# Optimization experiments

Measured on AMD Instinct MI355X. Metric: run time of the kernel, lower is better.

Reference implementation:

```python
import jax, jax.numpy as jnp
import numpy as np

B, T, D = 2, 1024, 2048
H, DK, DV = 32, 48, 96
KD, VD = H * DK, H * DV   # 1536, 3072
CS = 4
INTER = 5632
EPS = 1e-5


def rmsnorm(x, w, eps=EPS):
    return x * jax.lax.rsqrt(jnp.mean(x * x, axis=-1, keepdims=True) + eps) * w


def short_conv(x, w):
    # causal depthwise conv1d + silu; x [B,T,C], w [C,K]
    K = w.shape[1]
    xp = jnp.pad(x, ((0, 0), (K - 1, 0), (0, 0)))
    out = sum(xp[:, k:k + x.shape[1], :] * w[:, k] for k in range(K))
    return jax.nn.silu(out)


def l2norm(x, eps=1e-6):
    return x * jax.lax.rsqrt(jnp.sum(x * x, axis=-1, keepdims=True) + eps)


def gated_delta_rule(q, k, v, g, beta):
    # q,k [B,T,H,DK]; v [B,T,H,DV]; g,beta [B,T,H]
    scale = q.shape[-1] ** -0.5

    def step(S, inp):
        qt, kt, vt, gt, bt = inp
        S = S * jnp.exp(gt)[..., None, None]                    # decay state
        mem = jnp.einsum('bhk,bhkv->bhv', kt, S)                # retrieved value
        delta = (vt - mem) * bt[..., None]                      # beta-weighted error
        S = S + jnp.einsum('bhk,bhv->bhkv', kt, delta)          # rank-1 update
        o = jnp.einsum('bhk,bhkv->bhv', qt * scale, S)
        return S, o

    S0 = jnp.zeros((q.shape[0], q.shape[2], q.shape[3], v.shape[3]), q.dtype)
    xs = (q.transpose(1, 0, 2, 3), k.transpose(1, 0, 2, 3),
          v.transpose(1, 0, 2, 3), g.transpose(1, 0, 2), beta.transpose(1, 0, 2))
    _, o = jax.lax.scan(step, S0, xs)
    return o.transpose(1, 0, 2, 3)  # [B,T,H,DV]


def setup_inputs() -> dict:
    key = jax.random.key(0)
    ks = jax.random.split(key, 20)
    f = lambda k, sh, sc=0.02: jax.random.normal(k, sh, dtype=jnp.float32) * sc
    dt = jax.random.uniform(ks[7], (H,), minval=1e-3, maxval=0.1)
    return dict(
        x=jax.random.normal(ks[0], (B, T, D), dtype=jnp.float32),
        rms1_w=jnp.ones((D,), jnp.float32),
        rms2_w=jnp.ones((D,), jnp.float32),
        Wq=f(ks[1], (D, KD)), Wk=f(ks[2], (D, KD)), Wv=f(ks[3], (D, VD)),
        Wa=f(ks[4], (D, H)), Wb=f(ks[5], (D, H)), Wg=f(ks[6], (D, VD)),
        dt_bias=jnp.log(jnp.expm1(dt)),                         # softplus^-1(dt)
        A_log=jnp.log(jax.random.uniform(ks[8], (H,), minval=1.0, maxval=16.0)),
        conv_q_w=f(ks[9], (KD, CS), 0.5), conv_k_w=f(ks[10], (KD, CS), 0.5),
        conv_v_w=f(ks[11], (VD, CS), 0.5),
        gnorm_w=jnp.ones((DV,), jnp.float32),
        Wo=f(ks[12], (VD, D)),
        W1=f(ks[13], (D, INTER)), W3=f(ks[14], (D, INTER)), W2=f(ks[15], (INTER, D)),
    )


def reference(x, rms1_w, rms2_w, Wq, Wk, Wv, Wa, Wb, Wg, dt_bias, A_log,
              conv_q_w, conv_k_w, conv_v_w, gnorm_w, Wo, W1, W3, W2):
    b, t, _ = x.shape
    h = rmsnorm(x, rms1_w)
    # GatedDeltaNet
    q = short_conv(h @ Wq, conv_q_w).reshape(b, t, H, DK)
    k = short_conv(h @ Wk, conv_k_w).reshape(b, t, H, DK)
    v = short_conv(h @ Wv, conv_v_w).reshape(b, t, H, DV)
    q, k = l2norm(q), l2norm(k)
    g = -jnp.exp(A_log) * jax.nn.softplus(h @ Wa + dt_bias)    # [B,T,H] log-decay
    beta = jax.nn.sigmoid(h @ Wb)                              # [B,T,H]
    o = gated_delta_rule(q, k, v, g, beta)                     # [B,T,H,DV]
    gate = (h @ Wg).reshape(b, t, H, DV)
    o = rmsnorm(o, gnorm_w) * jax.nn.silu(gate)                # gated RMSNorm per head
    o = o.reshape(b, t, VD) @ Wo
    h2 = x + o
    # LLaMAMLP
    ff = rmsnorm(h2, rms2_w)
    out = h2 + (jax.nn.silu(ff @ W1) * (ff @ W3)) @ W2
    return out
```

## Files before the change

kernel.cpp:

```cpp
#include <hip/hip_runtime.h>
#include <math.h>

#define BB 2
#define TT 1024
#define DMODEL 2048
#define NH 32
#define DKH 48
#define DVH 96
#define KD 1536
#define VD 3072
#define INTER 5632
#define BT (BB*TT)

typedef unsigned short u16;
typedef __attribute__((ext_vector_type(8))) short bf16x8;
typedef __attribute__((ext_vector_type(4))) float f32x4;

__device__ __forceinline__ float siluf(float x) { return x / (1.f + __expf(-x)); }

__device__ __forceinline__ float bf2f(u16 u) {
    union { unsigned int i; float f; } v; v.i = ((unsigned int)u) << 16; return v.f;
}
__device__ __forceinline__ u16 f2bf(float f) {
    union { float f; unsigned int i; } v; v.f = f;
    unsigned int r = v.i + 0x7FFFu + ((v.i >> 16) & 1u);
    return (u16)(r >> 16);
}

__device__ __forceinline__ void async_copy16(const void* g, void* l) {
    __builtin_amdgcn_global_load_lds(
        (const __attribute__((address_space(1))) void*)g,
        (__attribute__((address_space(3))) void*)l, 16, 0, 0);
}

__global__ __launch_bounds__(256) void rmsnorm_kernel(
    const float* __restrict__ x, const float* __restrict__ w, u16* __restrict__ out)
{
    int m = blockIdx.x;
    int tid = threadIdx.x;
    const float4* xr = (const float4*)(x + (size_t)m * DMODEL);
    float4 a = xr[tid];
    float4 b = xr[tid + 256];
    float ss = a.x*a.x + a.y*a.y + a.z*a.z + a.w*a.w
             + b.x*b.x + b.y*b.y + b.z*b.z + b.w*b.w;
    #pragma unroll
    for (int off = 32; off; off >>= 1) ss += __shfl_xor(ss, off);
    __shared__ float wsum[4];
    if ((tid & 63) == 0) wsum[tid >> 6] = ss;
    __syncthreads();
    float tot = wsum[0] + wsum[1] + wsum[2] + wsum[3];
    float rn = rsqrtf(tot * (1.f / DMODEL) + 1e-5f);
    const float4* wr = (const float4*)w;
    float4 w0 = wr[tid], w1 = wr[tid + 256];
    ushort4 p0, p1;
    p0.x = f2bf(a.x*rn*w0.x); p0.y = f2bf(a.y*rn*w0.y);
    p0.z = f2bf(a.z*rn*w0.z); p0.w = f2bf(a.w*rn*w0.w);
    p1.x = f2bf(b.x*rn*w1.x); p1.y = f2bf(b.y*rn*w1.y);
    p1.z = f2bf(b.z*rn*w1.z); p1.w = f2bf(b.w*rn*w1.w);
    ushort4* orow = (ushort4*)(out + (size_t)m * DMODEL);
    orow[tid] = p0; orow[tid + 256] = p1;
}

__global__ __launch_bounds__(256) void transpose_cast(
    const float* __restrict__ in, u16* __restrict__ out, int K, int N)
{
    __shared__ float t[32][33];
    int bx = blockIdx.x;
    int by = blockIdx.y;
    int tx = threadIdx.x & 31, ty = threadIdx.x >> 5;
    #pragma unroll
    for (int r = ty; r < 32; r += 8)
        t[r][tx] = in[(size_t)(by * 32 + r) * N + bx * 32 + tx];
    __syncthreads();
    #pragma unroll
    for (int r = ty; r < 32; r += 8)
        out[(size_t)(bx * 32 + r) * K + by * 32 + tx] = f2bf(t[tx][r]);
}

template <int MODE>
__global__ __launch_bounds__(256) void gemm_bf16(
    const u16* __restrict__ A, const u16* __restrict__ Bt,
    void* __restrict__ Cv, const float* __restrict__ X,
    int M, int N, int K)
{
    __shared__ __align__(16) u16 As[128 * 32];
    __shared__ __align__(16) u16 Bs[128 * 32];
    int tid = threadIdx.x;
    int wave = tid >> 6, lane = tid & 63;
    int wr = wave >> 1, wc = wave & 1;
    int brow = blockIdx.y * 128, bcol = blockIdx.x * 128;
    int lr = lane & 15, lg = lane >> 4;

    f32x4 acc[4][4] = {};

    int ch0 = wave * 128 + lane;
    int ra0 = ch0 >> 2, pa0 = (ch0 & 3) * 8;
    int ch1 = ch0 + 64;
    int ra1 = ch1 >> 2, pa1 = (ch1 & 3) * 8;

    const u16* gA0 = A  + (size_t)(brow + ra0) * K + pa0;
    const u16* gA1 = A  + (size_t)(brow + ra1) * K + pa1;
    const u16* gB0 = Bt + (size_t)(bcol + ra0) * K + pa0;
    const u16* gB1 = Bt + (size_t)(bcol + ra1) * K + pa1;

    for (int kt = 0; kt < K; kt += 32) {
        __syncthreads();
        async_copy16(gA0 + kt, &As[ch0 * 8]);
        async_copy16(gA1 + kt, &As[ch1 * 8]);
        async_copy16(gB0 + kt, &Bs[ch0 * 8]);
        async_copy16(gB1 + kt, &Bs[ch1 * 8]);
        __syncthreads();

        bf16x8 aF[4], bF[4];
        #pragma unroll
        for (int m = 0; m < 4; m++)
            aF[m] = *(const bf16x8*)&As[(wr * 64 + m * 16 + lr) * 32 + lg * 8];
        #pragma unroll
        for (int n = 0; n < 4; n++)
            bF[n] = *(const bf16x8*)&Bs[(wc * 64 + n * 16 + lr) * 32 + lg * 8];
        #pragma unroll
        for (int m = 0; m < 4; m++)
            #pragma unroll
            for (int n = 0; n < 4; n++)
                acc[m][n] = __builtin_amdgcn_mfma_f32_16x16x32_bf16(
                    aF[m], bF[n], acc[m][n], 0, 0, 0);
    }

    int r0 = brow + wr * 64 + lg * 4;
    int c0 = bcol + wc * 64 + lr;
    #pragma unroll
    for (int m = 0; m < 4; m++) {
        #pragma unroll
        for (int n = 0; n < 4; n++) {
            #pragma unroll
            for (int r = 0; r < 4; r++) {
                size_t idx = (size_t)(r0 + m * 16 + r) * N + (c0 + n * 16);
                float v = acc[m][n][r];
                if (MODE == 0) {
                    ((float*)Cv)[idx] = v;
                } else if (MODE == 1) {
                    ((float*)Cv)[idx] = v + X[idx];
                } else {
                    ((u16*)Cv)[idx] = f2bf(v * siluf(X[idx]));
                }
            }
        }
    }
}

__global__ __launch_bounds__(256) void proj_gb_kernel(
    const u16* __restrict__ h, const float* __restrict__ Wa, const float* __restrict__ Wb,
    const float* __restrict__ dt_bias, const float* __restrict__ A_log,
    float* __restrict__ g, float* __restrict__ beta)
{
    int m = blockIdx.x, tid = threadIdx.x;
    __shared__ __align__(16) float hs[DMODEL];
    const uint4* hr = (const uint4*)(h + (size_t)m * DMODEL);
    uint4 hv = hr[tid];
    int base = tid * 8;
    hs[base + 0] = bf2f((u16)(hv.x & 0xffff)); hs[base + 1] = bf2f((u16)(hv.x >> 16));
    hs[base + 2] = bf2f((u16)(hv.y & 0xffff)); hs[base + 3] = bf2f((u16)(hv.y >> 16));
    hs[base + 4] = bf2f((u16)(hv.z & 0xffff)); hs[base + 5] = bf2f((u16)(hv.z >> 16));
    hs[base + 6] = bf2f((u16)(hv.w & 0xffff)); hs[base + 7] = bf2f((u16)(hv.w >> 16));
    __syncthreads();
    int out = tid >> 2;
    int part = tid & 3;
    int j = out & 31;
    const float* W = (out < 32) ? Wa : Wb;
    float s = 0.f;
    for (int kk = part; kk < DMODEL; kk += 4)
        s += hs[kk] * W[(size_t)kk * NH + j];
    s += __shfl_xor(s, 1);
    s += __shfl_xor(s, 2);
    if (part == 0) {
        if (out < 32) {
            float xx = s + dt_bias[j];
            float sp = (xx > 20.f) ? xx : log1pf(expf(xx));
            g[(size_t)m * NH + j] = -expf(A_log[j]) * sp;
        } else {
            beta[(size_t)m * NH + j] = 1.f / (1.f + expf(-s));
        }
    }
}

__global__ __launch_bounds__(256) void conv_qk_kernel(
    const float* __restrict__ pre, const float* __restrict__ w, float* __restrict__ out)
{
    int m = blockIdx.x;
    int b = m >> 10, t = m & 1023;
    int tid = threadIdx.x;
    int c0 = tid * 6;
    float o[6]; float ss = 0.f;
    #pragma unroll
    for (int jj = 0; jj < 6; jj++) {
        int c = c0 + jj;
        float acc = 0.f;
        #pragma unroll
        for (int kk = 0; kk < 4; kk++) {
            int tt = t - 3 + kk;
            if (tt >= 0)
                acc += pre[((size_t)(b * TT + tt)) * KD + c] * w[c * 4 + kk];
        }
        float s = siluf(acc);
        o[jj] = s; ss += s * s;
    }
    ss += __shfl_xor(ss, 1); ss += __shfl_xor(ss, 2); ss += __shfl_xor(ss, 4);
    float rn = rsqrtf(ss + 1e-6f);
    float* orow = out + (size_t)m * KD + c0;
    #pragma unroll
    for (int jj = 0; jj < 6; jj++) orow[jj] = o[jj] * rn;
}

__global__ __launch_bounds__(256) void conv_v_kernel(
    const float* __restrict__ pre, const float* __restrict__ w, float* __restrict__ out)
{
    int m = blockIdx.x;
    int b = m >> 10, t = m & 1023;
    int tid = threadIdx.x;
    int c0 = tid * 12;
    float* orow = out + (size_t)m * VD + c0;
    #pragma unroll
    for (int jj = 0; jj < 12; jj++) {
        int c = c0 + jj;
        float acc = 0.f;
        #pragma unroll
        for (int kk = 0; kk < 4; kk++) {
            int tt = t - 3 + kk;
            if (tt >= 0)
                acc += pre[((size_t)(b * TT + tt)) * VD + c] * w[c * 4 + kk];
        }
        orow[jj] = siluf(acc);
    }
}

#define SCH 32
__global__ __launch_bounds__(96) void scan_kernel(
    const float* __restrict__ q, const float* __restrict__ k, const float* __restrict__ v,
    const float* __restrict__ g, const float* __restrict__ beta, float* __restrict__ o)
{
    int bh = blockIdx.x;
    int b = bh >> 5, h = bh & 31;
    int tid = threadIdx.x;
    __shared__ __align__(16) float ks[SCH][DKH];
    __shared__ __align__(16) float qs[SCH][DKH];
    __shared__ __align__(16) float vs[SCH][DVH];
    __shared__ float gs[SCH], bs[SCH];
    float S[DKH];
    #pragma unroll
    for (int r = 0; r < DKH; r++) S[r] = 0.f;
    const float scale = 0.14433756729740643f;

    for (int t0 = 0; t0 < TT; t0 += SCH) {
        __syncthreads();
        for (int idx = tid; idx < SCH * DKH; idx += 96) {
            int ttc = idx / DKH, i = idx % DKH;
            size_t goff = ((size_t)(b * TT + t0 + ttc)) * KD + h * DKH + i;
            ks[ttc][i] = k[goff];
            qs[ttc][i] = q[goff];
        }
        for (int idx = tid; idx < SCH * DVH; idx += 96) {
            int ttc = idx / DVH, i = idx % DVH;
            vs[ttc][i] = v[((size_t)(b * TT + t0 + ttc)) * VD + h * DVH + i];
        }
        if (tid < SCH) {
            gs[tid] = g[(size_t)(b * TT + t0 + tid) * NH + h];
            bs[tid] = beta[(size_t)(b * TT + t0 + tid) * NH + h];
        }
        __syncthreads();

        for (int tc = 0; tc < SCH; tc++) {
            float eg = __expf(gs[tc]);
            float bt = bs[tc];
            float vt = vs[tc][tid];
            const float4* kv = (const float4*)&ks[tc][0];
            const float4* qv = (const float4*)&qs[tc][0];
            float4 kr[12];
            float m0 = 0.f, m1 = 0.f, m2 = 0.f, m3 = 0.f;
            #pragma unroll
            for (int r4 = 0; r4 < 12; r4++) {
                float4 kk4 = kv[r4];
                kr[r4] = kk4;
                S[4*r4+0] *= eg; m0 = fmaf(kk4.x, S[4*r4+0], m0);
                S[4*r4+1] *= eg; m1 = fmaf(kk4.y, S[4*r4+1], m1);
                S[4*r4+2] *= eg; m2 = fmaf(kk4.z, S[4*r4+2], m2);
                S[4*r4+3] *= eg; m3 = fmaf(kk4.w, S[4*r4+3], m3);
            }
            float delta = (vt - ((m0 + m1) + (m2 + m3))) * bt;
            float o0 = 0.f, o1 = 0.f, o2 = 0.f, o3 = 0.f;
            #pragma unroll
            for (int r4 = 0; r4 < 12; r4++) {
                float4 kk4 = kr[r4];
                float4 qq4 = qv[r4];
                S[4*r4+0] = fmaf(kk4.x, delta, S[4*r4+0]); o0 = fmaf(qq4.x, S[4*r4+0], o0);
                S[4*r4+1] = fmaf(kk4.y, delta, S[4*r4+1]); o1 = fmaf(qq4.y, S[4*r4+1], o1);
                S[4*r4+2] = fmaf(kk4.z, delta, S[4*r4+2]); o2 = fmaf(qq4.z, S[4*r4+2], o2);
                S[4*r4+3] = fmaf(kk4.w, delta, S[4*r4+3]); o3 = fmaf(qq4.w, S[4*r4+3], o3);
            }
            o[((size_t)(b * TT + t0 + tc)) * VD + h * DVH + tid] =
                ((o0 + o1) + (o2 + o3)) * scale;
        }
    }
}

__global__ __launch_bounds__(256) void gatednorm_kernel(
    const float* __restrict__ oraw, const float* __restrict__ gate,
    const float* __restrict__ gw, u16* __restrict__ out)
{
    int m = blockIdx.x, tid = threadIdx.x;
    int c0 = tid * 12;
    float o[12]; float ss = 0.f;
    const float* orow = oraw + (size_t)m * VD + c0;
    #pragma unroll
    for (int jj = 0; jj < 12; jj++) { float v_ = orow[jj]; o[jj] = v_; ss += v_ * v_; }
    ss += __shfl_xor(ss, 1); ss += __shfl_xor(ss, 2); ss += __shfl_xor(ss, 4);
    float rn = rsqrtf(ss * (1.f / 96.f) + 1e-5f);
    const float* grow = gate + (size_t)m * VD + c0;
    u16* outr = out + (size_t)m * VD + c0;
    int cw0 = c0 % 96;
    #pragma unroll
    for (int jj = 0; jj < 12; jj++) {
        float gt = grow[jj];
        outr[jj] = f2bf(o[jj] * rn * gw[cw0 + jj] * siluf(gt));
    }
}

extern "C" void kernel_launch(void* const* d_in, const int* in_sizes, int n_in,
                              void* d_out, int out_size, void* d_ws, size_t ws_size,
                              hipStream_t stream)
{
    const float* x        = (const float*)d_in[0];
    const float* rms1_w   = (const float*)d_in[1];
    const float* rms2_w   = (const float*)d_in[2];
    const float* Wq       = (const float*)d_in[3];
    const float* Wk       = (const float*)d_in[4];
    const float* Wv       = (const float*)d_in[5];
    const float* Wa       = (const float*)d_in[6];
    const float* Wb       = (const float*)d_in[7];
    const float* Wg       = (const float*)d_in[8];
    const float* dt_bias  = (const float*)d_in[9];
    const float* A_log    = (const float*)d_in[10];
    const float* conv_q_w = (const float*)d_in[11];
    const float* conv_k_w = (const float*)d_in[12];
    const float* conv_v_w = (const float*)d_in[13];
    const float* gnorm_w  = (const float*)d_in[14];
    const float* Wo       = (const float*)d_in[15];
    const float* W1       = (const float*)d_in[16];
    const float* W3       = (const float*)d_in[17];
    const float* W2       = (const float*)d_in[18];

    float* ws = (float*)d_ws;
    const size_t M1 = 1048576;
    u16*   wT    = (u16*)ws;
    u16*   h_bf  = (u16*)(ws + 11 * M1 / 2);
    float* qpre  = ws + 15 * M1 / 2;
    float* kpre  = ws + 21 * M1 / 2;
    float* vpre  = ws + 27 * M1 / 2;
    float* gate  = ws + 39 * M1 / 2;
    float* gbuf  = ws + 51 * M1 / 2;
    float* bbuf  = gbuf + 65536;
    float* qb    = ws + 103 * M1 / 4;
    float* kb    = ws + 115 * M1 / 4;
    float* vb    = ws + 127 * M1 / 4;
    float* oraw  = ws + 15 * M1 / 2;
    u16*   o2_bf = (u16*)(ws + 27 * M1 / 2);
    float* h2    = ws + 151 * M1 / 4;
    u16*   ff_bf = (u16*)(ws + 11 * M1 / 2);
    float* t1    = ws + 33 * M1 / 2;
    u16*   u_bf  = (u16*)(ws + 115 * M1 / 4);
    (void)ws_size; (void)n_in; (void)in_sizes; (void)out_size;

    rmsnorm_kernel<<<BT, 256, 0, stream>>>(x, rms1_w, h_bf);

    transpose_cast<<<dim3(KD/32, DMODEL/32), 256, 0, stream>>>(Wq, wT, DMODEL, KD);
    gemm_bf16<0><<<dim3(KD/128, BT/128), 256, 0, stream>>>(h_bf, wT, qpre, nullptr, BT, KD, DMODEL);
    transpose_cast<<<dim3(KD/32, DMODEL/32), 256, 0, stream>>>(Wk, wT, DMODEL, KD);
    gemm_bf16<0><<<dim3(KD/128, BT/128), 256, 0, stream>>>(h_bf, wT, kpre, nullptr, BT, KD, DMODEL);
    transpose_cast<<<dim3(VD/32, DMODEL/32), 256, 0, stream>>>(Wv, wT, DMODEL, VD);
    gemm_bf16<0><<<dim3(VD/128, BT/128), 256, 0, stream>>>(h_bf, wT, vpre, nullptr, BT, VD, DMODEL);
    transpose_cast<<<dim3(VD/32, DMODEL/32), 256, 0, stream>>>(Wg, wT, DMODEL, VD);
    gemm_bf16<0><<<dim3(VD/128, BT/128), 256, 0, stream>>>(h_bf, wT, gate, nullptr, BT, VD, DMODEL);
    proj_gb_kernel<<<BT, 256, 0, stream>>>(h_bf, Wa, Wb, dt_bias, A_log, gbuf, bbuf);

    conv_qk_kernel<<<BT, 256, 0, stream>>>(qpre, conv_q_w, qb);
    conv_qk_kernel<<<BT, 256, 0, stream>>>(kpre, conv_k_w, kb);
    conv_v_kernel<<<BT, 256, 0, stream>>>(vpre, conv_v_w, vb);

    scan_kernel<<<BB * NH, 96, 0, stream>>>(qb, kb, vb, gbuf, bbuf, oraw);

    gatednorm_kernel<<<BT, 256, 0, stream>>>(oraw, gate, gnorm_w, o2_bf);

    transpose_cast<<<dim3(DMODEL/32, VD/32), 256, 0, stream>>>(Wo, wT, VD, DMODEL);
    gemm_bf16<1><<<dim3(DMODEL/128, BT/128), 256, 0, stream>>>(o2_bf, wT, h2, x, BT, DMODEL, VD);

    rmsnorm_kernel<<<BT, 256, 0, stream>>>(h2, rms2_w, ff_bf);
    transpose_cast<<<dim3(INTER/32, DMODEL/32), 256, 0, stream>>>(W1, wT, DMODEL, INTER);
    gemm_bf16<0><<<dim3(INTER/128, BT/128), 256, 0, stream>>>(ff_bf, wT, t1, nullptr, BT, INTER, DMODEL);
    transpose_cast<<<dim3(INTER/32, DMODEL/32), 256, 0, stream>>>(W3, wT, DMODEL, INTER);
    gemm_bf16<2><<<dim3(INTER/128, BT/128), 256, 0, stream>>>(ff_bf, wT, u_bf, t1, BT, INTER, DMODEL);
    transpose_cast<<<dim3(DMODEL/32, INTER/32), 256, 0, stream>>>(W2, wT, INTER, DMODEL);
    gemm_bf16<1><<<dim3(DMODEL/128, BT/128), 256, 0, stream>>>(u_bf, wT, (float*)d_out, h2, BT, DMODEL, INTER);
}
```

Before: 2.183 ms.

## Split scan state across 4 lanes per value column with shuffle reductions

Result: faster. 1.786 ms (-18.2%).

```diff
diff --git a/kernel.cpp b/kernel.cpp
--- a/kernel.cpp
+++ b/kernel.cpp
@@ -234,70 +234,98 @@
 }
 
 #define SCH 32
-__global__ __launch_bounds__(96) void scan_kernel(
+__global__ __launch_bounds__(384) void scan_kernel(
     const float* __restrict__ q, const float* __restrict__ k, const float* __restrict__ v,
     const float* __restrict__ g, const float* __restrict__ beta, float* __restrict__ o)
 {
     int bh = blockIdx.x;
     int b = bh >> 5, h = bh & 31;
     int tid = threadIdx.x;
+    int lane = tid & 63;
+    int wave = tid >> 6;
+    int col  = wave * 16 + (lane >> 2);
+    int dkq  = lane & 3;
+    int r0   = dkq * 12;
+
     __shared__ __align__(16) float ks[SCH][DKH];
     __shared__ __align__(16) float qs[SCH][DKH];
     __shared__ __align__(16) float vs[SCH][DVH];
-    __shared__ float gs[SCH], bs[SCH];
-    float S[DKH];
-    #pragma unroll
-    for (int r = 0; r < DKH; r++) S[r] = 0.f;
+    __shared__ float egs[SCH], bs[SCH];
+
+    float S[12];
+    #pragma unroll
+    for (int i = 0; i < 12; i++) S[i] = 0.f;
     const float scale = 0.14433756729740643f;
+
+    const size_t kqbase = (size_t)(b * TT) * KD + h * DKH;
+    const size_t vbase  = (size_t)(b * TT) * VD + h * DVH;
 
     for (int t0 = 0; t0 < TT; t0 += SCH) {
         __syncthreads();
-        for (int idx = tid; idx < SCH * DKH; idx += 96) {
-            int ttc = idx / DKH, i = idx % DKH;
-            size_t goff = ((size_t)(b * TT + t0 + ttc)) * KD + h * DKH + i;
-            ks[ttc][i] = k[goff];
-            qs[ttc][i] = q[goff];
-        }
-        for (int idx = tid; idx < SCH * DVH; idx += 96) {
-            int ttc = idx / DVH, i = idx % DVH;
-            vs[ttc][i] = v[((size_t)(b * TT + t0 + ttc)) * VD + h * DVH + i];
+        #pragma unroll
+        for (int idx = tid; idx < SCH * DKH; idx += 384) {
+            int tt = idx / DKH, i = idx - tt * DKH;
+            size_t goff = kqbase + (size_t)(t0 + tt) * KD + i;
+            ks[tt][i] = k[goff];
+            qs[tt][i] = q[goff];
+        }
+        #pragma unroll
+        for (int idx = tid; idx < SCH * DVH; idx += 384) {
+            int tt = idx / DVH, i = idx - tt * DVH;
+            vs[tt][i] = v[vbase + (size_t)(t0 + tt) * VD + i];
         }
         if (tid < SCH) {
-            gs[tid] = g[(size_t)(b * TT + t0 + tid) * NH + h];
-            bs[tid] = beta[(size_t)(b * TT + t0 + tid) * NH + h];
+            egs[tid] = __expf(g[(size_t)(b * TT + t0 + tid) * NH + h]);
+            bs[tid]  = beta[(size_t)(b * TT + t0 + tid) * NH + h];
         }
         __syncthreads();
 
+        float4 kr[3], qr[3];
+        #pragma unroll
+        for (int j = 0; j < 3; j++) {
+            kr[j] = *(const float4*)&ks[0][r0 + j * 4];
+            qr[j] = *(const float4*)&qs[0][r0 + j * 4];
+        }
+        float vt = vs[0][col], eg = egs[0], bt = bs[0];
+
+        #pragma unroll
         for (int tc = 0; tc < SCH; tc++) {
-            float eg = __expf(gs[tc]);
-            float bt = bs[tc];
-            float vt = vs[tc][tid];
-            const float4* kv = (const float4*)&ks[tc][0];
-            const float4* qv = (const float4*)&qs[tc][0];
-            float4 kr[12];
-            float m0 = 0.f, m1 = 0.f, m2 = 0.f, m3 = 0.f;
+            float kk[12], qq[12];
+            *(float4*)&kk[0] = kr[0]; *(float4*)&kk[4] = kr[1]; *(float4*)&kk[8] = kr[2];
+            *(float4*)&qq[0] = qr[0]; *(float4*)&qq[4] = qr[1]; *(float4*)&qq[8] = qr[2];
+            float ceg = eg, cbt = bt, cvt = vt;
+            if (tc + 1 < SCH) {
+                #pragma unroll
+                for (int j = 0; j < 3; j++) {
+                    kr[j] = *(const float4*)&ks[tc + 1][r0 + j * 4];
+                    qr[j] = *(const float4*)&qs[tc + 1][r0 + j * 4];
+                }
+                vt = vs[tc + 1][col]; eg = egs[tc + 1]; bt = bs[tc + 1];
+            }
+            float d0 = kk[0] * S[0], d1 = kk[1] * S[1], d2 = kk[2] * S[2], d3 = kk[3] * S[3];
+            d0 = fmaf(kk[4], S[4], d0); d1 = fmaf(kk[5], S[5], d1);
+            d2 = fmaf(kk[6], S[6], d2); d3 = fmaf(kk[7], S[7], d3);
+            d0 = fmaf(kk[8], S[8], d0); d1 = fmaf(kk[9], S[9], d1);
+            d2 = fmaf(kk[10], S[10], d2); d3 = fmaf(kk[11], S[11], d3);
+            float dot = (d0 + d1) + (d2 + d3);
+            float es[12];
             #pragma unroll
-            for (int r4 = 0; r4 < 12; r4++) {
-                float4 kk4 = kv[r4];
-                kr[r4] = kk4;
-                S[4*r4+0] *= eg; m0 = fmaf(kk4.x, S[4*r4+0], m0);
-                S[4*r4+1] *= eg; m1 = fmaf(kk4.y, S[4*r4+1], m1);
-                S[4*r4+2] *= eg; m2 = fmaf(kk4.z, S[4*r4+2], m2);
-                S[4*r4+3] *= eg; m3 = fmaf(kk4.w, S[4*r4+3], m3);
-            }
-            float delta = (vt - ((m0 + m1) + (m2 + m3))) * bt;
-            float o0 = 0.f, o1 = 0.f, o2 = 0.f, o3 = 0.f;
+            for (int i = 0; i < 12; i++) es[i] = ceg * S[i];
+            dot += __shfl_xor(dot, 1);
+            dot += __shfl_xor(dot, 2);
+            float delta = (cvt - ceg * dot) * cbt;
             #pragma unroll
-            for (int r4 = 0; r4 < 12; r4++) {
-                float4 kk4 = kr[r4];
-                float4 qq4 = qv[r4];
-                S[4*r4+0] = fmaf(kk4.x, delta, S[4*r4+0]); o0 = fmaf(qq4.x, S[4*r4+0], o0);
-                S[4*r4+1] = fmaf(kk4.y, delta, S[4*r4+1]); o1 = fmaf(qq4.y, S[4*r4+1], o1);
-                S[4*r4+2] = fmaf(kk4.z, delta, S[4*r4+2]); o2 = fmaf(qq4.z, S[4*r4+2], o2);
-                S[4*r4+3] = fmaf(kk4.w, delta, S[4*r4+3]); o3 = fmaf(qq4.w, S[4*r4+3], o3);
-            }
-            o[((size_t)(b * TT + t0 + tc)) * VD + h * DVH + tid] =
-                ((o0 + o1) + (o2 + o3)) * scale;
+            for (int i = 0; i < 12; i++) S[i] = fmaf(kk[i], delta, es[i]);
+            float o0 = qq[0] * S[0], o1 = qq[1] * S[1], o2 = qq[2] * S[2], o3 = qq[3] * S[3];
+            o0 = fmaf(qq[4], S[4], o0); o1 = fmaf(qq[5], S[5], o1);
+            o2 = fmaf(qq[6], S[6], o2); o3 = fmaf(qq[7], S[7], o3);
+            o0 = fmaf(qq[8], S[8], o0); o1 = fmaf(qq[9], S[9], o1);
+            o2 = fmaf(qq[10], S[10], o2); o3 = fmaf(qq[11], S[11], o3);
+            float od = (o0 + o1) + (o2 + o3);
+            od += __shfl_xor(od, 1);
+            od += __shfl_xor(od, 2);
+            if (dkq == 0)
+                o[vbase + (size_t)(t0 + tc) * VD + col] = od * scale;
         }
     }
 }
@@ -385,7 +413,7 @@
     conv_qk_kernel<<<BT, 256, 0, stream>>>(kpre, conv_k_w, kb);
     conv_v_kernel<<<BT, 256, 0, stream>>>(vpre, conv_v_w, vb);
 
-    scan_kernel<<<BB * NH, 96, 0, stream>>>(qb, kb, vb, gbuf, bbuf, oraw);
+    scan_kernel<<<BB * NH, 384, 0, stream>>>(qb, kb, vb, gbuf, bbuf, oraw);
 
     gatednorm_kernel<<<BT, 256, 0, stream>>>(oraw, gate, gnorm_w, o2_bf);
 
```
